# Kernel optimization log

Measured on AMD Instinct MI355X. Metric: run time of the kernel, lower is better.

Reference implementation:

```python
import jax, jax.numpy as jnp
import numpy as np

B, F, D, H, E, K = 4, 2048, 1024, 2048, 8, 2  # batch, frames, dim, expert hidden, n_experts, top_k


def setup_inputs() -> dict:
    key = jax.random.key(0)
    ks = jax.random.split(key, 9)
    sc = lambda k, shape, fan_in: (jax.random.normal(k, shape, jnp.float32) * (fan_in ** -0.5))
    return {
        "x": jax.random.normal(ks[0], (B, F, D), jnp.float32),
        # router: Linear(D,D) -> SiLU -> Linear(D,E)
        "rw1": sc(ks[1], (D, D), D),
        "rb1": jnp.zeros((D,), jnp.float32),
        "rw2": sc(ks[2], (D, E), D),
        "rb2": jnp.zeros((E,), jnp.float32),
        # experts: E x (Linear(D,H) -> SiLU -> Linear(H,D))
        "ew1": sc(ks[3], (E, D, H), D),
        "eb1": jnp.zeros((E, H), jnp.float32),
        "ew2": sc(ks[4], (E, H, D), H),
        "eb2": jnp.zeros((E, D), jnp.float32),
    }


def reference(x, rw1, rb1, rw2, rb2, ew1, eb1, ew2, eb2):
    b, f, d = x.shape
    t = x.reshape(b * f, d)                                   # [T, D]
    # router (eval mode: no topk noise)
    logits = jax.nn.silu(t @ rw1 + rb1) @ rw2 + rb2            # [T, E]
    vals, idx = jax.lax.top_k(logits, K)                       # [T, K]
    rows = jnp.arange(t.shape[0])[:, None]
    masked = jnp.full_like(logits, -jnp.inf).at[rows, idx].set(vals)
    w = jax.nn.softmax(masked, axis=1)                         # [T, E], nonzero only on top-k
    # dense per-expert FFN, then weighted combine (residual: y starts as x)
    eh = jax.nn.silu(jnp.einsum('td,edh->teh', t, ew1) + eb1[None])   # [T, E, H]
    eo = jnp.einsum('teh,ehd->ted', eh, ew2) + eb2[None]              # [T, E, D]
    y = t + jnp.einsum('te,ted->td', w, eo)
    return y.reshape(b, f, d)
```

## Files before the change

### kernel.cpp

```cpp
#include <hip/hip_runtime.h>
#include <hip/hip_bf16.h>
#include <cstdint>
#include <cstddef>

#define T_TOK 8192
#define DDIM  1024
#define HDIM  2048
#define NEXP  8
#define TOPK  2
#define KAUG  (3 * DDIM)

typedef short bf16x8 __attribute__((ext_vector_type(8)));
typedef float f32x4  __attribute__((ext_vector_type(4)));

__device__ __forceinline__ unsigned short f2bf(float f) {
  union { float f; unsigned u; } v; v.f = f;
  unsigned r = v.u + 0x7FFFu + ((v.u >> 16) & 1u);
  return (unsigned short)(r >> 16);
}
__device__ __forceinline__ float bf2f(unsigned short h) {
  union { unsigned u; float f; } v; v.u = ((unsigned)h) << 16;
  return v.f;
}
__device__ __forceinline__ float silu_fast(float v) {
  return v / (1.0f + __expf(-v));
}
__device__ __forceinline__ float silu_precise(float v) {
  return v / (1.0f + expf(-v));
}

__device__ __forceinline__ void gload16(const unsigned short* g, unsigned short* l) {
  __builtin_amdgcn_global_load_lds(
      (const __attribute__((address_space(1))) unsigned int*)g,
      (__attribute__((address_space(3))) unsigned int*)l,
      16, 0, 0);
}

__global__ void split_x_kernel(const float* __restrict__ in,
                               unsigned short* __restrict__ xaug, int n4) {
  int i = blockIdx.x * blockDim.x + threadIdx.x;
  if (i >= n4) return;
  float4 v = ((const float4*)in)[i];
  int t = i / (DDIM / 4);
  int kc = (i % (DDIM / 4)) * 4;
  float f[4] = {v.x, v.y, v.z, v.w};
  ushort4 hi, lo;
  unsigned short h[4], l[4];
#pragma unroll
  for (int j = 0; j < 4; j++) {
    h[j] = f2bf(f[j]);
    l[j] = f2bf(f[j] - bf2f(h[j]));
  }
  hi.x = h[0]; hi.y = h[1]; hi.z = h[2]; hi.w = h[3];
  lo.x = l[0]; lo.y = l[1]; lo.z = l[2]; lo.w = l[3];
  *(ushort4*)&xaug[(size_t)t * KAUG + kc] = hi;
  *(ushort4*)&xaug[(size_t)t * KAUG + DDIM + kc] = hi;
  *(ushort4*)&xaug[(size_t)t * KAUG + 2 * DDIM + kc] = lo;
}

__global__ __launch_bounds__(256) void split_w_kernel(
    const float* __restrict__ in, unsigned short* __restrict__ waug) {
  __shared__ float tile[32][33];
  int c0 = blockIdx.x * 32, r0 = blockIdx.y * 32;
  int tx = threadIdx.x & 31, ty = threadIdx.x >> 5;
#pragma unroll
  for (int i = 0; i < 32; i += 8)
    tile[ty + i][tx] = in[(size_t)(r0 + ty + i) * DDIM + (c0 + tx)];
  __syncthreads();
#pragma unroll
  for (int i = 0; i < 32; i += 8) {
    float v = tile[tx][ty + i];
    unsigned short h = f2bf(v);
    unsigned short l = f2bf(v - bf2f(h));
    int n = c0 + ty + i, k = r0 + tx;
    waug[(size_t)n * KAUG + k] = h;
    waug[(size_t)n * KAUG + DDIM + k] = l;
    waug[(size_t)n * KAUG + 2 * DDIM + k] = h;
  }
}

__global__ __launch_bounds__(256) void transpose_conv_kernel(
    const float* __restrict__ in, unsigned short* __restrict__ out, int R, int C) {
  __shared__ float tile[32][33];
  const int z = blockIdx.z;
  const float* src = in + (size_t)z * R * C;
  unsigned short* dst = out + (size_t)z * R * C;
  int c0 = blockIdx.x * 32, r0 = blockIdx.y * 32;
  int tx = threadIdx.x & 31, ty = threadIdx.x >> 5;
#pragma unroll
  for (int i = 0; i < 32; i += 8)
    tile[ty + i][tx] = src[(size_t)(r0 + ty + i) * C + (c0 + tx)];
  __syncthreads();
#pragma unroll
  for (int i = 0; i < 32; i += 8)
    dst[(size_t)(c0 + ty + i) * R + (r0 + tx)] = f2bf(tile[tx][ty + i]);
}

__global__ void zero_small_kernel(int* __restrict__ counts, int* __restrict__ cursors) {
  int i = threadIdx.x;
  if (i < NEXP) { counts[i] = 0; cursors[i] = 0; }
}

template <int EPI, int BNT>
__global__ __launch_bounds__(512, 2) void gemm_mfma3(
    const unsigned short* __restrict__ Abase,
    const unsigned short* __restrict__ Btbase,
    const float* __restrict__ bias,
    float* __restrict__ outF,
    unsigned short* __restrict__ outBf,
    const int* __restrict__ toks,
    const int* __restrict__ offs, const int* __restrict__ cnts,
    int N, int KD, int Astride, int numE, int nTiles, int mCap) {
  constexpr int NI = BNT / 64;
  constexpr int RB = BNT / 128;
  constexpr int LPT = 2 + RB;
  constexpr int BUFB = 16384 + BNT * 64;
  extern __shared__ char sm[];

  const int id = blockIdx.x;
  const int e = id % numE;
  const int r = id / numE;
  const int n0 = (r % nTiles) * BNT;
  const int mb = r / nTiles;

  int ne = T_TOK, off = 0;
  if (EPI != 0) { ne = cnts[e]; off = offs[e]; }

  const unsigned short* Bt = Btbase + (size_t)e * N * KD;
  const unsigned short* A = (EPI == 2) ? (Abase + (size_t)off * Astride) : Abase;

  const int tid = threadIdx.x;
  const int lane = tid & 63, wid = tid >> 6;
  const int l16 = lane & 15, quad = lane >> 4;
  const int wm = wid >> 2, wn = wid & 3;

  const int rStage = tid >> 2;
  const int cS = (tid & 3) * 8;
  const int ldsW = wid << 10;

  const int NT = KD / 32;
  const int mStride = mCap * 256;

  const int aFragB = ((wm * 128 + l16) << 6) + (quad << 4);
  const int bFragB = 16384 + ((wn * (NI * 16) + l16) << 6) + (quad << 4);

  const unsigned short* bP[RB];
#pragma unroll
  for (int p = 0; p < RB; p++)
    bP[p] = Bt + (size_t)(n0 + p * 128 + rStage) * KD + cS;

  for (int m0 = mb * 256; m0 < ne; m0 += mStride) {
    const unsigned short* aP[2];
#pragma unroll
    for (int p = 0; p < 2; p++) {
      int row = m0 + p * 128 + rStage;
      int idx;
      if (EPI == 1) idx = toks[off + min(row, ne - 1)];
      else if (EPI == 2) idx = min(row, ne - 1);
      else idx = row;
      aP[p] = A + (size_t)idx * Astride + cS;
    }

    f32x4 acc[8][NI];
    const f32x4 zf = {0.f, 0.f, 0.f, 0.f};
#pragma unroll
    for (int mi = 0; mi < 8; mi++)
#pragma unroll
      for (int ni = 0; ni < NI; ni++) acc[mi][ni] = zf;

    auto stage = [&](int t, int b) {
      char* base = sm + b * BUFB + ldsW;
#pragma unroll
      for (int p = 0; p < 2; p++)
        gload16(aP[p] + t * 32, (unsigned short*)(base + p * 8192));
#pragma unroll
      for (int p = 0; p < RB; p++)
        gload16(bP[p] + t * 32, (unsigned short*)(base + 16384 + p * 8192));
    };

    stage(0, 0);
    stage(1, 1);
    stage(2, 2);

    for (int t = 0; t < NT; ++t) {
      if (t + 2 < NT)      __builtin_amdgcn_s_waitcnt(0x0F70 | (2 * LPT));
      else if (t + 1 < NT) __builtin_amdgcn_s_waitcnt(0x0F70 | LPT);
      else                 __builtin_amdgcn_s_waitcnt(0x0F70);
      __builtin_amdgcn_s_barrier();
      __builtin_amdgcn_sched_barrier(0);

      if (t + 3 < NT) stage(t + 3, (t + 3) & 3);

      const char* base = sm + (t & 3) * BUFB;
      bf16x8 av[8], bv[NI];
#pragma unroll
      for (int mi = 0; mi < 8; mi++)
        av[mi] = *(const bf16x8*)(base + aFragB + (mi << 10));
#pragma unroll
      for (int ni = 0; ni < NI; ni++)
        bv[ni] = *(const bf16x8*)(base + bFragB + (ni << 10));

      __builtin_amdgcn_s_setprio(1);
#pragma unroll
      for (int mi = 0; mi < 8; mi++)
#pragma unroll
        for (int ni = 0; ni < NI; ni++)
          acc[mi][ni] = __builtin_amdgcn_mfma_f32_16x16x32_bf16(
              av[mi], bv[ni], acc[mi][ni], 0, 0, 0);
      __builtin_amdgcn_s_setprio(0);
    }

    float bv4[NI];
#pragma unroll
    for (int ni = 0; ni < NI; ni++)
      bv4[ni] = bias[(size_t)e * N + n0 + wn * (NI * 16) + ni * 16 + l16];
#pragma unroll
    for (int mi = 0; mi < 8; mi++) {
      const int prow = m0 + wm * 128 + mi * 16 + quad * 4;
#pragma unroll
      for (int rr = 0; rr < 4; rr++) {
        const int p = prow + rr;
        if (EPI != 0 && p >= ne) continue;
#pragma unroll
        for (int ni = 0; ni < NI; ni++) {
          const int col = n0 + wn * (NI * 16) + ni * 16 + l16;
          float v = acc[mi][ni][rr] + bv4[ni];
          if (EPI == 0) {
            outF[(size_t)p * N + col] = silu_precise(v);
          } else if (EPI == 1) {
            outBf[(size_t)(off + p) * N + col] = f2bf(silu_fast(v));
          } else {
            outBf[(size_t)(off + p) * N + col] = f2bf(v);
          }
        }
      }
    }
  }
}

__global__ __launch_bounds__(256) void router2_kernel(
    const float* __restrict__ rh, const float* __restrict__ rw2,
    const float* __restrict__ rb2, float* __restrict__ logits) {
  int t = blockIdx.x * 4 + (threadIdx.x >> 6);
  int lane = threadIdx.x & 63;
  const float* row = rh + (size_t)t * DDIM;
  float acc[NEXP];
#pragma unroll
  for (int e = 0; e < NEXP; e++) acc[e] = 0.f;
  for (int k = lane; k < DDIM; k += 64) {
    float v = row[k];
    const float* w = rw2 + (size_t)k * NEXP;
#pragma unroll
    for (int e = 0; e < NEXP; e++) acc[e] += v * w[e];
  }
#pragma unroll
  for (int e = 0; e < NEXP; e++) {
#pragma unroll
    for (int off = 32; off > 0; off >>= 1) acc[e] += __shfl_xor(acc[e], off, 64);
  }
#pragma unroll
  for (int e = 0; e < NEXP; e++)
    if (lane == e) logits[(size_t)t * NEXP + e] = acc[e] + rb2[e];
}

__global__ void topk_kernel(const float* __restrict__ logits,
                            int* __restrict__ idx2, float* __restrict__ w2arr,
                            int* __restrict__ counts) {
  int t = blockIdx.x * blockDim.x + threadIdx.x;
  if (t >= T_TOK) return;
  float l[NEXP];
#pragma unroll
  for (int e = 0; e < NEXP; e++) l[e] = logits[(size_t)t * NEXP + e];
  int i1 = 0; float v1 = l[0];
#pragma unroll
  for (int e = 1; e < NEXP; e++)
    if (l[e] > v1) { v1 = l[e]; i1 = e; }
  int i2 = -1; float v2 = -3.4e38f;
#pragma unroll
  for (int e = 0; e < NEXP; e++)
    if (e != i1 && l[e] > v2) { v2 = l[e]; i2 = e; }
  float ex = expf(v2 - v1);
  float wa = 1.f / (1.f + ex);
  float wb = ex / (1.f + ex);
  idx2[t * 2] = i1; idx2[t * 2 + 1] = i2;
  w2arr[t * 2] = wa; w2arr[t * 2 + 1] = wb;
  atomicAdd(&counts[i1], 1);
  atomicAdd(&counts[i2], 1);
}

__global__ void prefix_kernel(const int* __restrict__ counts, int* __restrict__ offs) {
  if (threadIdx.x == 0 && blockIdx.x == 0) {
    int s = 0;
    for (int e = 0; e < NEXP; e++) { offs[e] = s; s += counts[e]; }
  }
}

__global__ void scatter_kernel(const int* __restrict__ idx2,
                               const int* __restrict__ offs, int* __restrict__ cursors,
                               int* __restrict__ toks, int* __restrict__ posArr) {
  int t = blockIdx.x * blockDim.x + threadIdx.x;
  if (t >= T_TOK) return;
#pragma unroll
  for (int j = 0; j < TOPK; j++) {
    int e = idx2[t * 2 + j];
    int pos = atomicAdd(&cursors[e], 1);
    int s = offs[e] + pos;
    toks[s] = t;
    posArr[t * 2 + j] = s;
  }
}

__global__ __launch_bounds__(256) void combine_kernel(
    const float* __restrict__ x, const unsigned short* __restrict__ eo,
    const int* __restrict__ posArr, const float* __restrict__ w2arr,
    float* __restrict__ y) {
  const int t = blockIdx.x;
  const int d = threadIdx.x * 4;
  const int s0 = posArr[t * 2], s1 = posArr[t * 2 + 1];
  const float w0 = w2arr[t * 2], w1 = w2arr[t * 2 + 1];
  float4 xv = *(const float4*)&x[(size_t)t * DDIM + d];
  ushort4 a = *(const ushort4*)&eo[(size_t)s0 * DDIM + d];
  ushort4 b = *(const ushort4*)&eo[(size_t)s1 * DDIM + d];
  float4 o;
  o.x = xv.x + w0 * bf2f(a.x) + w1 * bf2f(b.x);
  o.y = xv.y + w0 * bf2f(a.y) + w1 * bf2f(b.y);
  o.z = xv.z + w0 * bf2f(a.z) + w1 * bf2f(b.z);
  o.w = xv.w + w0 * bf2f(a.w) + w1 * bf2f(b.w);
  *(float4*)&y[(size_t)t * DDIM + d] = o;
}

extern "C" void kernel_launch(void* const* d_in, const int* in_sizes, int n_in,
                              void* d_out, int out_size, void* d_ws, size_t ws_size,
                              hipStream_t stream) {
  (void)in_sizes; (void)n_in; (void)out_size; (void)ws_size;
  const float* x   = (const float*)d_in[0];
  const float* rw1 = (const float*)d_in[1];
  const float* rb1 = (const float*)d_in[2];
  const float* rw2 = (const float*)d_in[3];
  const float* rb2 = (const float*)d_in[4];
  const float* ew1 = (const float*)d_in[5];
  const float* eb1 = (const float*)d_in[6];
  const float* ew2 = (const float*)d_in[7];
  const float* eb2 = (const float*)d_in[8];
  float* y = (float*)d_out;

  char* ws = (char*)d_ws;
  size_t o = 0;
  auto alloc = [&](size_t bytes) {
    size_t r = o;
    o += (bytes + 255) & ~(size_t)255;
    return r;
  };
  unsigned short* xaug  = (unsigned short*)(ws + alloc((size_t)T_TOK * KAUG * 2));
  unsigned short* waug  = (unsigned short*)(ws + alloc((size_t)DDIM * KAUG * 2));
  unsigned short* ew1t  = (unsigned short*)(ws + alloc((size_t)NEXP * HDIM * DDIM * 2));
  unsigned short* ew2t  = (unsigned short*)(ws + alloc((size_t)NEXP * DDIM * HDIM * 2));
  float*          rh    = (float*)(ws + alloc((size_t)T_TOK * DDIM * 4));
  float*          logits= (float*)(ws + alloc((size_t)T_TOK * NEXP * 4));
  int*            idx2  = (int*)(ws + alloc((size_t)T_TOK * 2 * 4));
  float*          w2    = (float*)(ws + alloc((size_t)T_TOK * 2 * 4));
  int*            toks  = (int*)(ws + alloc((size_t)T_TOK * TOPK * 4));
  int*            posArr= (int*)(ws + alloc((size_t)T_TOK * TOPK * 4));
  int*            counts= (int*)(ws + alloc(256));
  int*            cursors=(int*)(ws + alloc(256));
  int*            offs  = (int*)(ws + alloc(256));
  unsigned short* ehb   = (unsigned short*)(ws + alloc((size_t)T_TOK * TOPK * HDIM * 2));
  unsigned short* eo    = (unsigned short*)(ws + alloc((size_t)T_TOK * TOPK * DDIM * 2));

  constexpr int LDS_R = 4 * (16384 + 128 * 64);
  constexpr int LDS_E = 4 * (16384 + 256 * 64);
  static bool s_attr = false;
  if (!s_attr) {
    hipFuncSetAttribute((const void*)gemm_mfma3<0, 128>,
                        hipFuncAttributeMaxDynamicSharedMemorySize, LDS_R);
    hipFuncSetAttribute((const void*)gemm_mfma3<1, 256>,
                        hipFuncAttributeMaxDynamicSharedMemorySize, LDS_E);
    hipFuncSetAttribute((const void*)gemm_mfma3<2, 256>,
                        hipFuncAttributeMaxDynamicSharedMemorySize, LDS_E);
    s_attr = true;
  }

  zero_small_kernel<<<1, 64, 0, stream>>>(counts, cursors);

  const int n4 = T_TOK * DDIM / 4;
  split_x_kernel<<<(n4 + 255) / 256, 256, 0, stream>>>(x, xaug, n4);
  split_w_kernel<<<dim3(DDIM / 32, DDIM / 32), 256, 0, stream>>>(rw1, waug);
  transpose_conv_kernel<<<dim3(HDIM / 32, DDIM / 32, NEXP), 256, 0, stream>>>(ew1, ew1t, DDIM, HDIM);
  transpose_conv_kernel<<<dim3(DDIM / 32, HDIM / 32, NEXP), 256, 0, stream>>>(ew2, ew2t, HDIM, DDIM);

  gemm_mfma3<0, 128><<<256, 512, LDS_R, stream>>>(
      xaug, waug, rb1, rh, nullptr, nullptr, nullptr, nullptr,
      DDIM, KAUG, KAUG, 1, 8, 32);
  router2_kernel<<<T_TOK / 4, 256, 0, stream>>>(rh, rw2, rb2, logits);
  topk_kernel<<<T_TOK / 256, 256, 0, stream>>>(logits, idx2, w2, counts);
  prefix_kernel<<<1, 64, 0, stream>>>(counts, offs);
  scatter_kernel<<<T_TOK / 256, 256, 0, stream>>>(idx2, offs, cursors, toks, posArr);

  gemm_mfma3<1, 256><<<8 * 8 * 16, 512, LDS_E, stream>>>(
      xaug, ew1t, eb1, nullptr, ehb, toks, offs, counts,
      HDIM, DDIM, KAUG, NEXP, 8, 16);
  gemm_mfma3<2, 256><<<8 * 4 * 16, 512, LDS_E, stream>>>(
      ehb, ew2t, eb2, nullptr, eo, nullptr, offs, counts,
      DDIM, HDIM, HDIM, NEXP, 4, 16);
  combine_kernel<<<T_TOK, 256, 0, stream>>>(x, eo, posArr, w2, y);
}
```

Measured before the change: 739.6 us.

## Restructure MFMA GEMM to 128x256 tiles with K64 swizzled triple-buffered LDS

Replaces the templated GEMM with a fixed-shape kernel. Each block now computes a 128x256 output tile and consumes 64 K-elements per stage, instead of 256x{128,256} tiles with 32-wide K. LDS rows are XOR-swizzled to avoid bank conflicts on fragment reads. The pipeline goes from four buffers to three, and each K-step is split into two half-steps with barriers, so the next stage's loads are issued mid-iteration. The expert GEMMs lose M-tile reuse, and the extra barriers and larger LDS footprint (about 144KB per block) may limit overlap.

```diff
diff --git a/kernel.cpp b/kernel.cpp
--- a/kernel.cpp
+++ b/kernel.cpp
@@ -101,8 +101,8 @@
   if (i < NEXP) { counts[i] = 0; cursors[i] = 0; }
 }
 
-template <int EPI, int BNT>
-__global__ __launch_bounds__(512, 2) void gemm_mfma3(
+template <int EPI>
+__global__ __launch_bounds__(512, 2) void gemm_mfma4(
     const unsigned short* __restrict__ Abase,
     const unsigned short* __restrict__ Btbase,
     const float* __restrict__ bias,
@@ -111,16 +111,13 @@
     const int* __restrict__ toks,
     const int* __restrict__ offs, const int* __restrict__ cnts,
     int N, int KD, int Astride, int numE, int nTiles, int mCap) {
-  constexpr int NI = BNT / 64;
-  constexpr int RB = BNT / 128;
-  constexpr int LPT = 2 + RB;
-  constexpr int BUFB = 16384 + BNT * 64;
+  constexpr int BUFB = 49152;
   extern __shared__ char sm[];
 
   const int id = blockIdx.x;
   const int e = id % numE;
   const int r = id / numE;
-  const int n0 = (r % nTiles) * BNT;
+  const int n0 = (r % nTiles) * 256;
   const int mb = r / nTiles;
 
   int ne = T_TOK, off = 0;
@@ -134,48 +131,51 @@
   const int l16 = lane & 15, quad = lane >> 4;
   const int wm = wid >> 2, wn = wid & 3;
 
-  const int rStage = tid >> 2;
-  const int cS = (tid & 3) * 8;
+  const int rStage = tid >> 3;
+  const int cS8 = ((tid & 7) ^ (rStage & 7)) * 8;
   const int ldsW = wid << 10;
 
-  const int NT = KD / 32;
-  const int mStride = mCap * 256;
-
-  const int aFragB = ((wm * 128 + l16) << 6) + (quad << 4);
-  const int bFragB = 16384 + ((wn * (NI * 16) + l16) << 6) + (quad << 4);
-
-  const unsigned short* bP[RB];
-#pragma unroll
-  for (int p = 0; p < RB; p++)
-    bP[p] = Bt + (size_t)(n0 + p * 128 + rStage) * KD + cS;
-
-  for (int m0 = mb * 256; m0 < ne; m0 += mStride) {
+  const int NT = KD / 64;
+  const int mStride = mCap * 128;
+
+  const int sw = l16 & 7;
+  const int cOff0 = (quad ^ sw) << 4;
+  const int cOff1 = ((quad + 4) ^ sw) << 4;
+  const int aFragB = (wm * 64 + l16) << 7;
+  const int bFragB = 16384 + ((wn * 64 + l16) << 7);
+
+  const unsigned short* bP[4];
+#pragma unroll
+  for (int p = 0; p < 4; p++)
+    bP[p] = Bt + (size_t)(n0 + p * 64 + rStage) * KD + cS8;
+
+  for (int m0 = mb * 128; m0 < ne; m0 += mStride) {
     const unsigned short* aP[2];
 #pragma unroll
     for (int p = 0; p < 2; p++) {
-      int row = m0 + p * 128 + rStage;
+      int row = m0 + p * 64 + rStage;
       int idx;
       if (EPI == 1) idx = toks[off + min(row, ne - 1)];
       else if (EPI == 2) idx = min(row, ne - 1);
       else idx = row;
-      aP[p] = A + (size_t)idx * Astride + cS;
+      aP[p] = A + (size_t)idx * Astride + cS8;
     }
 
-    f32x4 acc[8][NI];
+    f32x4 acc[4][4];
     const f32x4 zf = {0.f, 0.f, 0.f, 0.f};
 #pragma unroll
-    for (int mi = 0; mi < 8; mi++)
-#pragma unroll
-      for (int ni = 0; ni < NI; ni++) acc[mi][ni] = zf;
+    for (int mi = 0; mi < 4; mi++)
+#pragma unroll
+      for (int ni = 0; ni < 4; ni++) acc[mi][ni] = zf;
 
     auto stage = [&](int t, int b) {
       char* base = sm + b * BUFB + ldsW;
-#pragma unroll
-      for (int p = 0; p < 2; p++)
-        gload16(aP[p] + t * 32, (unsigned short*)(base + p * 8192));
-#pragma unroll
-      for (int p = 0; p < RB; p++)
-        gload16(bP[p] + t * 32, (unsigned short*)(base + 16384 + p * 8192));
+      gload16(aP[0] + t * 64, (unsigned short*)(base));
+      gload16(aP[1] + t * 64, (unsigned short*)(base + 8192));
+      gload16(bP[0] + t * 64, (unsigned short*)(base + 16384));
+      gload16(bP[1] + t * 64, (unsigned short*)(base + 24576));
+      gload16(bP[2] + t * 64, (unsigned short*)(base + 32768));
+      gload16(bP[3] + t * 64, (unsigned short*)(base + 40960));
     };
 
     stage(0, 0);
@@ -183,47 +183,66 @@
     stage(2, 2);
 
     for (int t = 0; t < NT; ++t) {
-      if (t + 2 < NT)      __builtin_amdgcn_s_waitcnt(0x0F70 | (2 * LPT));
-      else if (t + 1 < NT) __builtin_amdgcn_s_waitcnt(0x0F70 | LPT);
+      const char* base = sm + (t % 3) * BUFB;
+      if (t + 2 < NT)      __builtin_amdgcn_s_waitcnt(0x0F70 | 12);
+      else if (t + 1 < NT) __builtin_amdgcn_s_waitcnt(0x0F70 | 6);
       else                 __builtin_amdgcn_s_waitcnt(0x0F70);
       __builtin_amdgcn_s_barrier();
       __builtin_amdgcn_sched_barrier(0);
 
-      if (t + 3 < NT) stage(t + 3, (t + 3) & 3);
-
-      const char* base = sm + (t & 3) * BUFB;
-      bf16x8 av[8], bv[NI];
-#pragma unroll
-      for (int mi = 0; mi < 8; mi++)
-        av[mi] = *(const bf16x8*)(base + aFragB + (mi << 10));
-#pragma unroll
-      for (int ni = 0; ni < NI; ni++)
-        bv[ni] = *(const bf16x8*)(base + bFragB + (ni << 10));
-
+      bf16x8 av[4], bv[4];
+#pragma unroll
+      for (int mi = 0; mi < 4; mi++)
+        av[mi] = *(const bf16x8*)(base + aFragB + (mi << 11) + cOff0);
+#pragma unroll
+      for (int ni = 0; ni < 4; ni++)
+        bv[ni] = *(const bf16x8*)(base + bFragB + (ni << 11) + cOff0);
+      __builtin_amdgcn_s_waitcnt(0xC07F);
+      __builtin_amdgcn_sched_barrier(0);
       __builtin_amdgcn_s_setprio(1);
 #pragma unroll
-      for (int mi = 0; mi < 8; mi++)
-#pragma unroll
-        for (int ni = 0; ni < NI; ni++)
+      for (int mi = 0; mi < 4; mi++)
+#pragma unroll
+        for (int ni = 0; ni < 4; ni++)
+          acc[mi][ni] = __builtin_amdgcn_mfma_f32_16x16x32_bf16(
+              av[mi], bv[ni], acc[mi][ni], 0, 0, 0);
+      __builtin_amdgcn_s_setprio(0);
+      __builtin_amdgcn_s_barrier();
+
+#pragma unroll
+      for (int mi = 0; mi < 4; mi++)
+        av[mi] = *(const bf16x8*)(base + aFragB + (mi << 11) + cOff1);
+#pragma unroll
+      for (int ni = 0; ni < 4; ni++)
+        bv[ni] = *(const bf16x8*)(base + bFragB + (ni << 11) + cOff1);
+      __builtin_amdgcn_s_waitcnt(0xC07F);
+      __builtin_amdgcn_s_barrier();
+      __builtin_amdgcn_sched_barrier(0);
+      if (t + 3 < NT) stage(t + 3, t % 3);
+      __builtin_amdgcn_s_setprio(1);
+#pragma unroll
+      for (int mi = 0; mi < 4; mi++)
+#pragma unroll
+        for (int ni = 0; ni < 4; ni++)
           acc[mi][ni] = __builtin_amdgcn_mfma_f32_16x16x32_bf16(
               av[mi], bv[ni], acc[mi][ni], 0, 0, 0);
       __builtin_amdgcn_s_setprio(0);
     }
 
-    float bv4[NI];
-#pragma unroll
-    for (int ni = 0; ni < NI; ni++)
-      bv4[ni] = bias[(size_t)e * N + n0 + wn * (NI * 16) + ni * 16 + l16];
-#pragma unroll
-    for (int mi = 0; mi < 8; mi++) {
-      const int prow = m0 + wm * 128 + mi * 16 + quad * 4;
+    float bv4[4];
+#pragma unroll
+    for (int ni = 0; ni < 4; ni++)
+      bv4[ni] = bias[(size_t)e * N + n0 + wn * 64 + ni * 16 + l16];
+#pragma unroll
+    for (int mi = 0; mi < 4; mi++) {
+      const int prow = m0 + wm * 64 + mi * 16 + quad * 4;
 #pragma unroll
       for (int rr = 0; rr < 4; rr++) {
         const int p = prow + rr;
         if (EPI != 0 && p >= ne) continue;
 #pragma unroll
-        for (int ni = 0; ni < NI; ni++) {
-          const int col = n0 + wn * (NI * 16) + ni * 16 + l16;
+        for (int ni = 0; ni < 4; ni++) {
+          const int col = n0 + wn * 64 + ni * 16 + l16;
           float v = acc[mi][ni][rr] + bv4[ni];
           if (EPI == 0) {
             outF[(size_t)p * N + col] = silu_precise(v);
@@ -367,16 +386,15 @@
   unsigned short* ehb   = (unsigned short*)(ws + alloc((size_t)T_TOK * TOPK * HDIM * 2));
   unsigned short* eo    = (unsigned short*)(ws + alloc((size_t)T_TOK * TOPK * DDIM * 2));
 
-  constexpr int LDS_R = 4 * (16384 + 128 * 64);
-  constexpr int LDS_E = 4 * (16384 + 256 * 64);
+  constexpr int LDS_SZ = 3 * 49152;
   static bool s_attr = false;
   if (!s_attr) {
-    hipFuncSetAttribute((const void*)gemm_mfma3<0, 128>,
-                        hipFuncAttributeMaxDynamicSharedMemorySize, LDS_R);
-    hipFuncSetAttribute((const void*)gemm_mfma3<1, 256>,
-                        hipFuncAttributeMaxDynamicSharedMemorySize, LDS_E);
-    hipFuncSetAttribute((const void*)gemm_mfma3<2, 256>,
-                        hipFuncAttributeMaxDynamicSharedMemorySize, LDS_E);
+    (void)hipFuncSetAttribute((const void*)gemm_mfma4<0>,
+                              hipFuncAttributeMaxDynamicSharedMemorySize, LDS_SZ);
+    (void)hipFuncSetAttribute((const void*)gemm_mfma4<1>,
+                              hipFuncAttributeMaxDynamicSharedMemorySize, LDS_SZ);
+    (void)hipFuncSetAttribute((const void*)gemm_mfma4<2>,
+                              hipFuncAttributeMaxDynamicSharedMemorySize, LDS_SZ);
     s_attr = true;
   }
 
@@ -388,18 +406,18 @@
   transpose_conv_kernel<<<dim3(HDIM / 32, DDIM / 32, NEXP), 256, 0, stream>>>(ew1, ew1t, DDIM, HDIM);
   transpose_conv_kernel<<<dim3(DDIM / 32, HDIM / 32, NEXP), 256, 0, stream>>>(ew2, ew2t, HDIM, DDIM);
 
-  gemm_mfma3<0, 128><<<256, 512, LDS_R, stream>>>(
+  gemm_mfma4<0><<<256, 512, LDS_SZ, stream>>>(
       xaug, waug, rb1, rh, nullptr, nullptr, nullptr, nullptr,
-      DDIM, KAUG, KAUG, 1, 8, 32);
+      DDIM, KAUG, KAUG, 1, 4, 64);
   router2_kernel<<<T_TOK / 4, 256, 0, stream>>>(rh, rw2, rb2, logits);
   topk_kernel<<<T_TOK / 256, 256, 0, stream>>>(logits, idx2, w2, counts);
   prefix_kernel<<<1, 64, 0, stream>>>(counts, offs);
   scatter_kernel<<<T_TOK / 256, 256, 0, stream>>>(idx2, offs, cursors, toks, posArr);
 
-  gemm_mfma3<1, 256><<<8 * 8 * 16, 512, LDS_E, stream>>>(
+  gemm_mfma4<1><<<8 * 8 * 16, 512, LDS_SZ, stream>>>(
       xaug, ew1t, eb1, nullptr, ehb, toks, offs, counts,
       HDIM, DDIM, KAUG, NEXP, 8, 16);
-  gemm_mfma3<2, 256><<<8 * 4 * 16, 512, LDS_E, stream>>>(
+  gemm_mfma4<2><<<8 * 4 * 16, 512, LDS_SZ, stream>>>(
       ehb, ew2t, eb2, nullptr, eo, nullptr, offs, counts,
       DDIM, HDIM, HDIM, NEXP, 4, 16);
   combine_kernel<<<T_TOK, 256, 0, stream>>>(x, eo, posArr, w2, y);
```

Result: no change. 747.6 us (+1.1%).
